# Performance work log

Hardware: AMD Instinct MI355X
Metric: run time of the kernel (lower is better)

Reference implementation:

```python
import jax, jax.numpy as jnp
import numpy as np

N_NODES = 100000
N_EDGES = 1250000
D_IN = 32
H = 64
EPS = 1e-5


def layer_norm(x, g, b):
    mu = jnp.mean(x, axis=-1, keepdims=True)
    var = jnp.mean(jnp.square(x - mu), axis=-1, keepdims=True)
    return (x - mu) * jax.lax.rsqrt(var + EPS) * g + b


def setup_inputs() -> dict:
    key = jax.random.key(0)
    ks = jax.random.split(key, 6)
    x = jax.random.normal(ks[0], (N_NODES, D_IN), dtype=jnp.float32)
    edge_index = jax.random.randint(ks[1], (2, N_EDGES), 0, N_NODES, dtype=jnp.int64)
    W1 = jax.random.normal(ks[2], (D_IN, H), dtype=jnp.float32) * (1.0 / np.sqrt(D_IN))
    b1 = jax.random.normal(ks[3], (H,), dtype=jnp.float32) * 0.01
    W2 = jax.random.normal(ks[4], (H, H), dtype=jnp.float32) * (1.0 / np.sqrt(H))
    b2 = jax.random.normal(ks[5], (H,), dtype=jnp.float32) * 0.01
    g1 = jnp.ones((H,), dtype=jnp.float32)
    beta1 = jnp.zeros((H,), dtype=jnp.float32)
    g2 = jnp.ones((H,), dtype=jnp.float32)
    beta2 = jnp.zeros((H,), dtype=jnp.float32)
    return {"x": x, "edge_index": edge_index, "W1": W1, "b1": b1, "g1": g1,
            "beta1": beta1, "W2": W2, "b2": b2, "g2": g2, "beta2": beta2}


def reference(x, edge_index, W1, b1, g1, beta1, W2, b2, g2, beta2):
    # node MLP: Linear -> LN -> ReLU, twice
    h = jax.nn.relu(layer_norm(x @ W1 + b1, g1, beta1))
    h = jax.nn.relu(layer_norm(h @ W2 + b2, g2, beta2))
    # message passing: gather source features, scatter-add to destinations
    row, col = edge_index[0], edge_index[1]
    aggr = jax.ops.segment_sum(h[col], row, num_segments=N_NODES)  # [N, H]
    return h + aggr
```

## Files before the change

kernel.cpp:

```cpp
#include <hip/hip_runtime.h>

#define N_NODES 100000
#define D_IN 32
#define H 64
#define EPS 1e-5f
#define RSTR 32
#define CAP 32
#define OV_CAP 32768

typedef float floatx2 __attribute__((ext_vector_type(2)));

__device__ __forceinline__ unsigned short f2bf(float f) {
    union { float f; unsigned int u; } c; c.f = f;
    unsigned int b = c.u + 0x7FFFu + ((c.u >> 16) & 1u);
    return (unsigned short)(b >> 16);
}
__device__ __forceinline__ float bf2f(unsigned short s) {
    union { unsigned int u; float f; } c; c.u = ((unsigned int)s) << 16;
    return c.f;
}

__global__ __launch_bounds__(256, 2) void fused_kernel(
    const float* __restrict__ x,
    const float* __restrict__ W1, const float* __restrict__ b1,
    const float* __restrict__ g1, const float* __restrict__ be1,
    const float* __restrict__ W2, const float* __restrict__ b2,
    const float* __restrict__ g2, const float* __restrict__ be2,
    unsigned short* __restrict__ hb, unsigned char* __restrict__ hb8,
    const int* __restrict__ ei, int* __restrict__ cnt, int* __restrict__ bkt,
    int* __restrict__ ovCnt, int2* __restrict__ ov,
    int E, int SB, int TOT)
{
    const int i = blockIdx.x;
    const int before = (int)((long long)i * SB / TOT);
    const int after  = (int)((long long)(i + 1) * SB / TOT);

    if (after > before) {
        int t = before * 256 + threadIdx.x;
        int e0 = t * 8;
        if (e0 >= E) return;

        int rows[8], cols[8], pos[8];
        if (e0 + 7 < E) {
            int4 r0 = *(const int4*)(ei + e0);
            int4 r1 = *(const int4*)(ei + e0 + 4);
            int4 c0 = *(const int4*)(ei + E + e0);
            int4 c1 = *(const int4*)(ei + E + e0 + 4);
            rows[0]=r0.x; rows[1]=r0.y; rows[2]=r0.z; rows[3]=r0.w;
            rows[4]=r1.x; rows[5]=r1.y; rows[6]=r1.z; rows[7]=r1.w;
            cols[0]=c0.x; cols[1]=c0.y; cols[2]=c0.z; cols[3]=c0.w;
            cols[4]=c1.x; cols[5]=c1.y; cols[6]=c1.z; cols[7]=c1.w;
        } else {
#pragma unroll
            for (int j = 0; j < 8; ++j) {
                int e = e0 + j;
                if (e < E) { rows[j] = ei[e]; cols[j] = ei[E + e]; }
                else rows[j] = -1;
            }
        }
#pragma unroll
        for (int j = 0; j < 8; ++j)
            if (rows[j] >= 0) pos[j] = atomicAdd(&cnt[rows[j]], 1);
#pragma unroll
        for (int j = 0; j < 8; ++j) {
            if (rows[j] < 0) continue;
            if (pos[j] < CAP) {
                __builtin_nontemporal_store(cols[j], &bkt[rows[j] * RSTR + pos[j]]);
            } else {
                int s = atomicAdd(ovCnt, 1);
                if (s < OV_CAP) ov[s] = make_int2(rows[j], cols[j]);
            }
        }
        return;
    }

    int gid = (i - before) * 256 + threadIdx.x;
    int node = gid < N_NODES ? gid : N_NODES - 1;

    float xr[D_IN];
    {
        const float4* xp = (const float4*)(x + (long long)node * D_IN);
#pragma unroll
        for (int i2 = 0; i2 < D_IN / 4; ++i2) {
            float4 v = xp[i2];
            xr[4*i2+0] = v.x; xr[4*i2+1] = v.y; xr[4*i2+2] = v.z; xr[4*i2+3] = v.w;
        }
    }

    float h1[H];
#pragma unroll
    for (int jb = 0; jb < H / 4; ++jb) {
        float4 b = *(const float4*)(b1 + jb * 4);
        h1[4*jb+0] = b.x; h1[4*jb+1] = b.y; h1[4*jb+2] = b.z; h1[4*jb+3] = b.w;
    }
#pragma unroll
    for (int k = 0; k < D_IN; ++k) {
        float xk = xr[k];
#pragma unroll
        for (int jb = 0; jb < H / 4; ++jb) {
            float4 w = *(const float4*)(W1 + k * H + jb * 4);
            h1[4*jb+0] += xk * w.x; h1[4*jb+1] += xk * w.y;
            h1[4*jb+2] += xk * w.z; h1[4*jb+3] += xk * w.w;
        }
    }
    {
        float s0=0,s1=0,s2=0,s3=0, q0=0,q1=0,q2=0,q3=0;
#pragma unroll
        for (int j = 0; j < H; j += 4) {
            s0 += h1[j+0]; s1 += h1[j+1]; s2 += h1[j+2]; s3 += h1[j+3];
            q0 += h1[j+0]*h1[j+0]; q1 += h1[j+1]*h1[j+1];
            q2 += h1[j+2]*h1[j+2]; q3 += h1[j+3]*h1[j+3];
        }
        float mu  = (s0+s1+s2+s3) * (1.0f / H);
        float var = (q0+q1+q2+q3) * (1.0f / H) - mu * mu;
        float rs  = rsqrtf(var + EPS);
#pragma unroll
        for (int jb = 0; jb < H / 4; ++jb) {
            float4 g = *(const float4*)(g1 + jb * 4);
            float4 be = *(const float4*)(be1 + jb * 4);
            h1[4*jb+0] = fmaxf((h1[4*jb+0]-mu)*rs*g.x + be.x, 0.0f);
            h1[4*jb+1] = fmaxf((h1[4*jb+1]-mu)*rs*g.y + be.y, 0.0f);
            h1[4*jb+2] = fmaxf((h1[4*jb+2]-mu)*rs*g.z + be.z, 0.0f);
            h1[4*jb+3] = fmaxf((h1[4*jb+3]-mu)*rs*g.w + be.w, 0.0f);
        }
    }

    float h2[H];
#pragma unroll
    for (int jb = 0; jb < H / 4; ++jb) {
        float4 b = *(const float4*)(b2 + jb * 4);
        h2[4*jb+0] = b.x; h2[4*jb+1] = b.y; h2[4*jb+2] = b.z; h2[4*jb+3] = b.w;
    }
#pragma unroll
    for (int k = 0; k < H; ++k) {
        float hk = h1[k];
#pragma unroll
        for (int jb = 0; jb < H / 4; ++jb) {
            float4 w = *(const float4*)(W2 + k * H + jb * 4);
            h2[4*jb+0] += hk * w.x; h2[4*jb+1] += hk * w.y;
            h2[4*jb+2] += hk * w.z; h2[4*jb+3] += hk * w.w;
        }
    }
    {
        float s0=0,s1=0,s2=0,s3=0, q0=0,q1=0,q2=0,q3=0;
#pragma unroll
        for (int j = 0; j < H; j += 4) {
            s0 += h2[j+0]; s1 += h2[j+1]; s2 += h2[j+2]; s3 += h2[j+3];
            q0 += h2[j+0]*h2[j+0]; q1 += h2[j+1]*h2[j+1];
            q2 += h2[j+2]*h2[j+2]; q3 += h2[j+3]*h2[j+3];
        }
        float mu  = (s0+s1+s2+s3) * (1.0f / H);
        float var = (q0+q1+q2+q3) * (1.0f / H) - mu * mu;
        float rs  = rsqrtf(var + EPS);

        unsigned short* hp = hb + (long long)node * H;
        unsigned int w8[H / 4];
#pragma unroll
        for (int jb = 0; jb < H / 4; ++jb) {
            float4 g = *(const float4*)(g2 + jb * 4);
            float4 be = *(const float4*)(be2 + jb * 4);
            float4 v;
            v.x = fmaxf((h2[4*jb+0]-mu)*rs*g.x + be.x, 0.0f);
            v.y = fmaxf((h2[4*jb+1]-mu)*rs*g.y + be.y, 0.0f);
            v.z = fmaxf((h2[4*jb+2]-mu)*rs*g.z + be.z, 0.0f);
            v.w = fmaxf((h2[4*jb+3]-mu)*rs*g.w + be.w, 0.0f);
            ushort4 u;
            u.x = f2bf(v.x); u.y = f2bf(v.y); u.z = f2bf(v.z); u.w = f2bf(v.w);
            *(ushort4*)(hp + 4*jb) = u;
            int lo = __builtin_amdgcn_cvt_pk_fp8_f32(v.x, v.y, 0, false);
            w8[jb] = (unsigned int)__builtin_amdgcn_cvt_pk_fp8_f32(v.z, v.w, lo, true);
        }
        unsigned int* hp8 = (unsigned int*)(hb8 + (long long)node * H);
#pragma unroll
        for (int q = 0; q < H / 16; ++q)
            *(uint4*)(hp8 + q * 4) = make_uint4(w8[4*q+0], w8[4*q+1], w8[4*q+2], w8[4*q+3]);
    }
}

__global__ __launch_bounds__(256, 2) void aggr_kernel(
    const int* __restrict__ cnt, const int* __restrict__ bkt,
    const unsigned short* __restrict__ hb, const unsigned char* __restrict__ hb8,
    float* __restrict__ out,
    const int* __restrict__ ovCnt, const int2* __restrict__ ov)
{
    const int t    = threadIdx.x & 63;
    const int sub  = t >> 4;
    const int l    = t & 15;
    const int q    = l & 3;
    const int g    = l >> 2;
    const int wave = blockIdx.x * 4 + (threadIdx.x >> 6);
    const int node = wave * 4 + sub;

    int m = cnt[node];
    if (m > CAP) m = CAP;
    const int base = node * RSTR;

    int4 ea = *(const int4*)(bkt + base + g * 8);
    int4 eb = *(const int4*)(bkt + base + g * 8 + 4);
    int ed[8] = { ea.x, ea.y, ea.z, ea.w, eb.x, eb.y, eb.z, eb.w };

    const uint4* h84 = (const uint4*)hb8;
    const int e0 = g * 8;

    float s[16];
#pragma unroll
    for (int j = 0; j < 16; ++j) s[j] = 0.f;

    uint4 vv[8];
#pragma unroll
    for (int k = 0; k < 8; ++k)
        if (e0 + k < m) vv[k] = h84[(ed[k] << 2) + q];

#pragma unroll
    for (int k = 0; k < 8; ++k) {
        if (e0 + k < m) {
            unsigned int w[4] = { vv[k].x, vv[k].y, vv[k].z, vv[k].w };
#pragma unroll
            for (int u = 0; u < 4; ++u) {
                floatx2 p0 = __builtin_amdgcn_cvt_pk_f32_fp8(w[u], false);
                floatx2 p1 = __builtin_amdgcn_cvt_pk_f32_fp8(w[u], true);
                s[4*u+0] += p0.x; s[4*u+1] += p0.y;
                s[4*u+2] += p1.x; s[4*u+3] += p1.y;
            }
        }
    }

#pragma unroll
    for (int j = 0; j < 16; ++j) {
        s[j] += __shfl_xor(s[j], 4, 64);
        s[j] += __shfl_xor(s[j], 8, 64);
    }

    const int co = q * 16 + g * 4;
    float a0 = s[g*4+0], a1 = s[g*4+1], a2 = s[g*4+2], a3 = s[g*4+3];

    {
        uint2 sv = *(const uint2*)(hb + ((long long)node << 6) + co);
        a0 += bf2f((unsigned short)(sv.x & 0xFFFFu));
        a1 += bf2f((unsigned short)(sv.x >> 16));
        a2 += bf2f((unsigned short)(sv.y & 0xFFFFu));
        a3 += bf2f((unsigned short)(sv.y >> 16));
    }

    int nov = *ovCnt; if (nov > OV_CAP) nov = OV_CAP;
    for (int i = 0; i < nov; ++i) {
        int2 rc = ov[i];
        if (rc.x == node) {
            uint2 vvо = *(const uint2*)(hb + ((long long)rc.y << 6) + co);
            a0 += bf2f((unsigned short)(vvо.x & 0xFFFFu));
            a1 += bf2f((unsigned short)(vvо.x >> 16));
            a2 += bf2f((unsigned short)(vvо.y & 0xFFFFu));
            a3 += bf2f((unsigned short)(vvо.y >> 16));
        }
    }

    *(float4*)(out + ((long long)node << 6) + co) = make_float4(a0, a1, a2, a3);
}

extern "C" void kernel_launch(void* const* d_in, const int* in_sizes, int n_in,
                              void* d_out, int out_size, void* d_ws, size_t ws_size,
                              hipStream_t stream)
{
    const float* x   = (const float*)d_in[0];
    const int*   ei  = (const int*)d_in[1];
    const float* W1  = (const float*)d_in[2];
    const float* b1  = (const float*)d_in[3];
    const float* g1  = (const float*)d_in[4];
    const float* be1 = (const float*)d_in[5];
    const float* W2  = (const float*)d_in[6];
    const float* b2  = (const float*)d_in[7];
    const float* g2  = (const float*)d_in[8];
    const float* be2 = (const float*)d_in[9];

    float* out = (float*)d_out;

    char* ws = (char*)d_ws;
    unsigned short* hb    = (unsigned short*)ws;
    unsigned char*  hb8   = (unsigned char*)(ws + 12800000);
    int*            cnt   = (int*)(ws + 19200000);
    int*            ovCnt = (int*)(ws + 19600000);
    int2*           ov    = (int2*)(ws + 19600064);
    int*            bkt   = (int*)(ws + 19862208);

    const int E = in_sizes[1] / 2;

    (void)hipMemsetAsync(cnt, 0, 400064, stream);

    const int SB = ((E + 7) / 8 + 255) / 256;
    const int MB = (N_NODES + 255) / 256;
    fused_kernel<<<SB + MB, 256, 0, stream>>>(
        x, W1, b1, g1, be1, W2, b2, g2, be2, hb, hb8,
        ei, cnt, bkt, ovCnt, ov, E, SB, SB + MB);

    aggr_kernel<<<N_NODES / 16, 256, 0, stream>>>(cnt, bkt, hb, hb8, out, ovCnt, ov);
}
```

Baseline: 205.9 us.

## Split aggregation into two source-range passes to shrink gathered working set

Aggregation now runs as two launches. Each launch gathers only edges whose source node falls in half of the node range, so the fp8 feature table being read randomly is about half as large per pass and is more likely to stay cache-resident. The first pass writes partial sums plus the self term to the output. The second pass reads those back and adds the other half and the overflow edges. In exchange, the bucket lists are read twice, the output makes an extra write and read round trip, and there is a second launch.

```diff
diff --git a/kernel.cpp b/kernel.cpp
--- a/kernel.cpp
+++ b/kernel.cpp
@@ -7,6 +7,7 @@
 #define RSTR 32
 #define CAP 32
 #define OV_CAP 32768
+#define SRC_HALF 50000
 
 typedef float floatx2 __attribute__((ext_vector_type(2)));
 
@@ -177,11 +178,12 @@
     }
 }
 
-__global__ __launch_bounds__(256, 2) void aggr_kernel(
+__global__ __launch_bounds__(256, 2) void aggr_pass_kernel(
     const int* __restrict__ cnt, const int* __restrict__ bkt,
     const unsigned short* __restrict__ hb, const unsigned char* __restrict__ hb8,
     float* __restrict__ out,
-    const int* __restrict__ ovCnt, const int2* __restrict__ ov)
+    const int* __restrict__ ovCnt, const int2* __restrict__ ov,
+    int srcLo, int srcHi, int isFinal)
 {
     const int t    = threadIdx.x & 63;
     const int sub  = t >> 4;
@@ -198,9 +200,14 @@
     int4 ea = *(const int4*)(bkt + base + g * 8);
     int4 eb = *(const int4*)(bkt + base + g * 8 + 4);
     int ed[8] = { ea.x, ea.y, ea.z, ea.w, eb.x, eb.y, eb.z, eb.w };
+    const int e0 = g * 8;
+
+    bool keep[8];
+#pragma unroll
+    for (int k = 0; k < 8; ++k)
+        keep[k] = (e0 + k < m) && (ed[k] >= srcLo) && (ed[k] < srcHi);
 
     const uint4* h84 = (const uint4*)hb8;
-    const int e0 = g * 8;
 
     float s[16];
 #pragma unroll
@@ -209,11 +216,11 @@
     uint4 vv[8];
 #pragma unroll
     for (int k = 0; k < 8; ++k)
-        if (e0 + k < m) vv[k] = h84[(ed[k] << 2) + q];
+        if (keep[k]) vv[k] = h84[(ed[k] << 2) + q];
 
 #pragma unroll
     for (int k = 0; k < 8; ++k) {
-        if (e0 + k < m) {
+        if (keep[k]) {
             unsigned int w[4] = { vv[k].x, vv[k].y, vv[k].z, vv[k].w };
 #pragma unroll
             for (int u = 0; u < 4; ++u) {
@@ -234,23 +241,26 @@
     const int co = q * 16 + g * 4;
     float a0 = s[g*4+0], a1 = s[g*4+1], a2 = s[g*4+2], a3 = s[g*4+3];
 
-    {
+    if (!isFinal) {
         uint2 sv = *(const uint2*)(hb + ((long long)node << 6) + co);
         a0 += bf2f((unsigned short)(sv.x & 0xFFFFu));
         a1 += bf2f((unsigned short)(sv.x >> 16));
         a2 += bf2f((unsigned short)(sv.y & 0xFFFFu));
         a3 += bf2f((unsigned short)(sv.y >> 16));
-    }
-
-    int nov = *ovCnt; if (nov > OV_CAP) nov = OV_CAP;
-    for (int i = 0; i < nov; ++i) {
-        int2 rc = ov[i];
-        if (rc.x == node) {
-            uint2 vvо = *(const uint2*)(hb + ((long long)rc.y << 6) + co);
-            a0 += bf2f((unsigned short)(vvо.x & 0xFFFFu));
-            a1 += bf2f((unsigned short)(vvо.x >> 16));
-            a2 += bf2f((unsigned short)(vvо.y & 0xFFFFu));
-            a3 += bf2f((unsigned short)(vvо.y >> 16));
+    } else {
+        float4 prev = *(const float4*)(out + ((long long)node << 6) + co);
+        a0 += prev.x; a1 += prev.y; a2 += prev.z; a3 += prev.w;
+
+        int nov = *ovCnt; if (nov > OV_CAP) nov = OV_CAP;
+        for (int i = 0; i < nov; ++i) {
+            int2 rc = ov[i];
+            if (rc.x == node) {
+                uint2 vo = *(const uint2*)(hb + ((long long)rc.y << 6) + co);
+                a0 += bf2f((unsigned short)(vo.x & 0xFFFFu));
+                a1 += bf2f((unsigned short)(vo.x >> 16));
+                a2 += bf2f((unsigned short)(vo.y & 0xFFFFu));
+                a3 += bf2f((unsigned short)(vo.y >> 16));
+            }
         }
     }
 
@@ -292,5 +302,8 @@
         x, W1, b1, g1, be1, W2, b2, g2, be2, hb, hb8,
         ei, cnt, bkt, ovCnt, ov, E, SB, SB + MB);
 
-    aggr_kernel<<<N_NODES / 16, 256, 0, stream>>>(cnt, bkt, hb, hb8, out, ovCnt, ov);
-}
+    aggr_pass_kernel<<<N_NODES / 16, 256, 0, stream>>>(
+        cnt, bkt, hb, hb8, out, ovCnt, ov, 0, SRC_HALF, 0);
+    aggr_pass_kernel<<<N_NODES / 16, 256, 0, stream>>>(
+        cnt, bkt, hb, hb8, out, ovCnt, ov, SRC_HALF, N_NODES, 1);
+}
```

Measured after the change: 222.5 us. 8.1% more time.

## Split edge bucketing by destination half to overlap with aggregation

Applied to the files above, without the earlier changes.

Edge bucketing is split by destination-row range into two passes. The first pass (rows below 50000) runs alongside the node MLP. The second pass (upper rows) runs in the same kernel that aggregates the lower half of nodes, and a third kernel aggregates the upper half. This is meant to overlap scatter atomics with gather work and shorten the dependency chain; in exchange the full edge list is read twice and one more kernel launch is added. Lower-half aggregation reads the overflow count while upper-half scatter may still be appending entries, which could pick up stale overflow records.

```diff
diff --git a/kernel.cpp b/kernel.cpp
--- a/kernel.cpp
+++ b/kernel.cpp
@@ -7,6 +7,7 @@
 #define RSTR 32
 #define CAP 32
 #define OV_CAP 32768
+#define HALF 50000
 
 typedef float floatx2 __attribute__((ext_vector_type(2)));
 
@@ -20,7 +21,130 @@
     return c.f;
 }
 
-__global__ __launch_bounds__(256, 2) void fused_kernel(
+__device__ __forceinline__ void scatter_range(
+    const int* __restrict__ ei, int* __restrict__ cnt, int* __restrict__ bkt,
+    int* __restrict__ ovCnt, int2* __restrict__ ov,
+    int E, int chunk, int lo, int hi)
+{
+    int t = chunk * 256 + threadIdx.x;
+    int e0 = t * 8;
+    if (e0 >= E) return;
+
+    int rows[8], cols[8], pos[8];
+    if (e0 + 7 < E) {
+        int4 r0 = *(const int4*)(ei + e0);
+        int4 r1 = *(const int4*)(ei + e0 + 4);
+        int4 c0 = *(const int4*)(ei + E + e0);
+        int4 c1 = *(const int4*)(ei + E + e0 + 4);
+        rows[0]=r0.x; rows[1]=r0.y; rows[2]=r0.z; rows[3]=r0.w;
+        rows[4]=r1.x; rows[5]=r1.y; rows[6]=r1.z; rows[7]=r1.w;
+        cols[0]=c0.x; cols[1]=c0.y; cols[2]=c0.z; cols[3]=c0.w;
+        cols[4]=c1.x; cols[5]=c1.y; cols[6]=c1.z; cols[7]=c1.w;
+    } else {
+#pragma unroll
+        for (int j = 0; j < 8; ++j) {
+            int e = e0 + j;
+            if (e < E) { rows[j] = ei[e]; cols[j] = ei[E + e]; }
+            else rows[j] = -1;
+        }
+    }
+#pragma unroll
+    for (int j = 0; j < 8; ++j) {
+        pos[j] = -1;
+        if (rows[j] >= lo && rows[j] < hi)
+            pos[j] = atomicAdd(&cnt[rows[j]], 1);
+    }
+#pragma unroll
+    for (int j = 0; j < 8; ++j) {
+        if (pos[j] < 0) continue;
+        if (pos[j] < CAP) {
+            __builtin_nontemporal_store(cols[j], &bkt[rows[j] * RSTR + pos[j]]);
+        } else {
+            int s = atomicAdd(ovCnt, 1);
+            if (s < OV_CAP) ov[s] = make_int2(rows[j], cols[j]);
+        }
+    }
+}
+
+__device__ __forceinline__ void aggr_node(
+    const int* __restrict__ cnt, const int* __restrict__ bkt,
+    const unsigned short* __restrict__ hb, const unsigned char* __restrict__ hb8,
+    float* __restrict__ out,
+    const int* __restrict__ ovCnt, const int2* __restrict__ ov,
+    int node)
+{
+    const int t = threadIdx.x & 63;
+    const int l = t & 15;
+    const int q = l & 3;
+    const int g = l >> 2;
+
+    int m = cnt[node];
+    if (m > CAP) m = CAP;
+    const int base = node * RSTR;
+
+    int4 ea = *(const int4*)(bkt + base + g * 8);
+    int4 eb = *(const int4*)(bkt + base + g * 8 + 4);
+    int ed[8] = { ea.x, ea.y, ea.z, ea.w, eb.x, eb.y, eb.z, eb.w };
+    const int e0 = g * 8;
+
+    const uint4* h84 = (const uint4*)hb8;
+
+    float s[16];
+#pragma unroll
+    for (int j = 0; j < 16; ++j) s[j] = 0.f;
+
+    uint4 vv[8];
+#pragma unroll
+    for (int k = 0; k < 8; ++k)
+        if (e0 + k < m) vv[k] = h84[(ed[k] << 2) + q];
+
+#pragma unroll
+    for (int k = 0; k < 8; ++k) {
+        if (e0 + k < m) {
+            unsigned int w[4] = { vv[k].x, vv[k].y, vv[k].z, vv[k].w };
+#pragma unroll
+            for (int u = 0; u < 4; ++u) {
+                floatx2 p0 = __builtin_amdgcn_cvt_pk_f32_fp8(w[u], false);
+                floatx2 p1 = __builtin_amdgcn_cvt_pk_f32_fp8(w[u], true);
+                s[4*u+0] += p0.x; s[4*u+1] += p0.y;
+                s[4*u+2] += p1.x; s[4*u+3] += p1.y;
+            }
+        }
+    }
+
+#pragma unroll
+    for (int j = 0; j < 16; ++j) {
+        s[j] += __shfl_xor(s[j], 4, 64);
+        s[j] += __shfl_xor(s[j], 8, 64);
+    }
+
+    const int co = q * 16 + g * 4;
+    float a0 = s[g*4+0], a1 = s[g*4+1], a2 = s[g*4+2], a3 = s[g*4+3];
+
+    {
+        uint2 sv = *(const uint2*)(hb + ((long long)node << 6) + co);
+        a0 += bf2f((unsigned short)(sv.x & 0xFFFFu));
+        a1 += bf2f((unsigned short)(sv.x >> 16));
+        a2 += bf2f((unsigned short)(sv.y & 0xFFFFu));
+        a3 += bf2f((unsigned short)(sv.y >> 16));
+    }
+
+    int nov = *ovCnt; if (nov > OV_CAP) nov = OV_CAP;
+    for (int i = 0; i < nov; ++i) {
+        int2 rc = ov[i];
+        if (rc.x == node) {
+            uint2 vo = *(const uint2*)(hb + ((long long)rc.y << 6) + co);
+            a0 += bf2f((unsigned short)(vo.x & 0xFFFFu));
+            a1 += bf2f((unsigned short)(vo.x >> 16));
+            a2 += bf2f((unsigned short)(vo.y & 0xFFFFu));
+            a3 += bf2f((unsigned short)(vo.y >> 16));
+        }
+    }
+
+    *(float4*)(out + ((long long)node << 6) + co) = make_float4(a0, a1, a2, a3);
+}
+
+__global__ __launch_bounds__(256, 2) void k1_kernel(
     const float* __restrict__ x,
     const float* __restrict__ W1, const float* __restrict__ b1,
     const float* __restrict__ g1, const float* __restrict__ be1,
@@ -36,41 +160,7 @@
     const int after  = (int)((long long)(i + 1) * SB / TOT);
 
     if (after > before) {
-        int t = before * 256 + threadIdx.x;
-        int e0 = t * 8;
-        if (e0 >= E) return;
-
-        int rows[8], cols[8], pos[8];
-        if (e0 + 7 < E) {
-            int4 r0 = *(const int4*)(ei + e0);
-            int4 r1 = *(const int4*)(ei + e0 + 4);
-            int4 c0 = *(const int4*)(ei + E + e0);
-            int4 c1 = *(const int4*)(ei + E + e0 + 4);
-            rows[0]=r0.x; rows[1]=r0.y; rows[2]=r0.z; rows[3]=r0.w;
-            rows[4]=r1.x; rows[5]=r1.y; rows[6]=r1.z; rows[7]=r1.w;
-            cols[0]=c0.x; cols[1]=c0.y; cols[2]=c0.z; cols[3]=c0.w;
-            cols[4]=c1.x; cols[5]=c1.y; cols[6]=c1.z; cols[7]=c1.w;
-        } else {
-#pragma unroll
-            for (int j = 0; j < 8; ++j) {
-                int e = e0 + j;
-                if (e < E) { rows[j] = ei[e]; cols[j] = ei[E + e]; }
-                else rows[j] = -1;
-            }
-        }
-#pragma unroll
-        for (int j = 0; j < 8; ++j)
-            if (rows[j] >= 0) pos[j] = atomicAdd(&cnt[rows[j]], 1);
-#pragma unroll
-        for (int j = 0; j < 8; ++j) {
-            if (rows[j] < 0) continue;
-            if (pos[j] < CAP) {
-                __builtin_nontemporal_store(cols[j], &bkt[rows[j] * RSTR + pos[j]]);
-            } else {
-                int s = atomicAdd(ovCnt, 1);
-                if (s < OV_CAP) ov[s] = make_int2(rows[j], cols[j]);
-            }
-        }
+        scatter_range(ei, cnt, bkt, ovCnt, ov, E, before, 0, HALF);
         return;
     }
 
@@ -177,7 +267,30 @@
     }
 }
 
-__global__ __launch_bounds__(256, 2) void aggr_kernel(
+__global__ __launch_bounds__(256, 2) void k2_kernel(
+    const unsigned short* __restrict__ hb, const unsigned char* __restrict__ hb8,
+    const int* __restrict__ ei, int* __restrict__ cnt, int* __restrict__ bkt,
+    int* __restrict__ ovCnt, int2* __restrict__ ov,
+    float* __restrict__ out,
+    int E, int SB, int TOT)
+{
+    const int i = blockIdx.x;
+    const int before = (int)((long long)i * SB / TOT);
+    const int after  = (int)((long long)(i + 1) * SB / TOT);
+
+    if (after > before) {
+        scatter_range(ei, cnt, bkt, ovCnt, ov, E, before, HALF, N_NODES);
+        return;
+    }
+
+    const int t    = threadIdx.x & 63;
+    const int sub  = t >> 4;
+    const int wave = (i - before) * 4 + (threadIdx.x >> 6);
+    const int node = wave * 4 + sub;
+    aggr_node(cnt, bkt, hb, hb8, out, ovCnt, ov, node);
+}
+
+__global__ __launch_bounds__(256, 2) void k3_kernel(
     const int* __restrict__ cnt, const int* __restrict__ bkt,
     const unsigned short* __restrict__ hb, const unsigned char* __restrict__ hb8,
     float* __restrict__ out,
@@ -185,76 +298,9 @@
 {
     const int t    = threadIdx.x & 63;
     const int sub  = t >> 4;
-    const int l    = t & 15;
-    const int q    = l & 3;
-    const int g    = l >> 2;
     const int wave = blockIdx.x * 4 + (threadIdx.x >> 6);
-    const int node = wave * 4 + sub;
-
-    int m = cnt[node];
-    if (m > CAP) m = CAP;
-    const int base = node * RSTR;
-
-    int4 ea = *(const int4*)(bkt + base + g * 8);
-    int4 eb = *(const int4*)(bkt + base + g * 8 + 4);
-    int ed[8] = { ea.x, ea.y, ea.z, ea.w, eb.x, eb.y, eb.z, eb.w };
-
-    const uint4* h84 = (const uint4*)hb8;
-    const int e0 = g * 8;
-
-    float s[16];
-#pragma unroll
-    for (int j = 0; j < 16; ++j) s[j] = 0.f;
-
-    uint4 vv[8];
-#pragma unroll
-    for (int k = 0; k < 8; ++k)
-        if (e0 + k < m) vv[k] = h84[(ed[k] << 2) + q];
-
-#pragma unroll
-    for (int k = 0; k < 8; ++k) {
-        if (e0 + k < m) {
-            unsigned int w[4] = { vv[k].x, vv[k].y, vv[k].z, vv[k].w };
-#pragma unroll
-            for (int u = 0; u < 4; ++u) {
-                floatx2 p0 = __builtin_amdgcn_cvt_pk_f32_fp8(w[u], false);
-                floatx2 p1 = __builtin_amdgcn_cvt_pk_f32_fp8(w[u], true);
-                s[4*u+0] += p0.x; s[4*u+1] += p0.y;
-                s[4*u+2] += p1.x; s[4*u+3] += p1.y;
-            }
-        }
-    }
-
-#pragma unroll
-    for (int j = 0; j < 16; ++j) {
-        s[j] += __shfl_xor(s[j], 4, 64);
-        s[j] += __shfl_xor(s[j], 8, 64);
-    }
-
-    const int co = q * 16 + g * 4;
-    float a0 = s[g*4+0], a1 = s[g*4+1], a2 = s[g*4+2], a3 = s[g*4+3];
-
-    {
-        uint2 sv = *(const uint2*)(hb + ((long long)node << 6) + co);
-        a0 += bf2f((unsigned short)(sv.x & 0xFFFFu));
-        a1 += bf2f((unsigned short)(sv.x >> 16));
-        a2 += bf2f((unsigned short)(sv.y & 0xFFFFu));
-        a3 += bf2f((unsigned short)(sv.y >> 16));
-    }
-
-    int nov = *ovCnt; if (nov > OV_CAP) nov = OV_CAP;
-    for (int i = 0; i < nov; ++i) {
-        int2 rc = ov[i];
-        if (rc.x == node) {
-            uint2 vvо = *(const uint2*)(hb + ((long long)rc.y << 6) + co);
-            a0 += bf2f((unsigned short)(vvо.x & 0xFFFFu));
-            a1 += bf2f((unsigned short)(vvо.x >> 16));
-            a2 += bf2f((unsigned short)(vvо.y & 0xFFFFu));
-            a3 += bf2f((unsigned short)(vvо.y >> 16));
-        }
-    }
-
-    *(float4*)(out + ((long long)node << 6) + co) = make_float4(a0, a1, a2, a3);
+    const int node = HALF + wave * 4 + sub;
+    aggr_node(cnt, bkt, hb, hb8, out, ovCnt, ov, node);
 }
 
 extern "C" void kernel_launch(void* const* d_in, const int* in_sizes, int n_in,
@@ -286,11 +332,16 @@
 
     (void)hipMemsetAsync(cnt, 0, 400064, stream);
 
-    const int SB = ((E + 7) / 8 + 255) / 256;
-    const int MB = (N_NODES + 255) / 256;
-    fused_kernel<<<SB + MB, 256, 0, stream>>>(
+    const int SB  = ((E + 7) / 8 + 255) / 256;
+    const int MB  = (N_NODES + 255) / 256;
+    const int AB  = HALF / 16;
+
+    k1_kernel<<<SB + MB, 256, 0, stream>>>(
         x, W1, b1, g1, be1, W2, b2, g2, be2, hb, hb8,
         ei, cnt, bkt, ovCnt, ov, E, SB, SB + MB);
 
-    aggr_kernel<<<N_NODES / 16, 256, 0, stream>>>(cnt, bkt, hb, hb8, out, ovCnt, ov);
-}
+    k2_kernel<<<SB + AB, 256, 0, stream>>>(
+        hb, hb8, ei, cnt, bkt, ovCnt, ov, out, E, SB, SB + AB);
+
+    k3_kernel<<<AB, 256, 0, stream>>>(cnt, bkt, hb, hb8, out, ovCnt, ov);
+}
```

Measured after the change: 212.0 us. 3.0% more time.

## Replace global per-row atomic bucketing with two-pass binned partition via shared memory

Applied to the files above, without the earlier changes.

Edges are first partitioned into 196 coarse bins of 512 rows, using shared-memory histograms and one global atomic per bin per block. They are written as packed (local row, col) words. A new kernel then builds each bin's per-row buckets in LDS and streams them out coalesced. This replaces 1.25M scattered global atomics and scattered bucket stores, at the cost of an extra kernel launch, an extra pass over the partition buffer, and a large LDS footprint (about 66KB per block) that limits occupancy of the new kernel.

```diff
diff --git a/kernel.cpp b/kernel.cpp
--- a/kernel.cpp
+++ b/kernel.cpp
@@ -7,6 +7,9 @@
 #define RSTR 32
 #define CAP 32
 #define OV_CAP 32768
+#define NBINS 196
+#define BINSZ 512
+#define BINCAP 7168
 
 typedef float floatx2 __attribute__((ext_vector_type(2)));
 
@@ -20,14 +23,14 @@
     return c.f;
 }
 
-__global__ __launch_bounds__(256, 2) void fused_kernel(
+__global__ __launch_bounds__(256, 2) void ka_kernel(
     const float* __restrict__ x,
     const float* __restrict__ W1, const float* __restrict__ b1,
     const float* __restrict__ g1, const float* __restrict__ be1,
     const float* __restrict__ W2, const float* __restrict__ b2,
     const float* __restrict__ g2, const float* __restrict__ be2,
     unsigned short* __restrict__ hb, unsigned char* __restrict__ hb8,
-    const int* __restrict__ ei, int* __restrict__ cnt, int* __restrict__ bkt,
+    const int* __restrict__ ei, int* __restrict__ part, int* __restrict__ binCur,
     int* __restrict__ ovCnt, int2* __restrict__ ov,
     int E, int SB, int TOT)
 {
@@ -36,11 +39,13 @@
     const int after  = (int)((long long)(i + 1) * SB / TOT);
 
     if (after > before) {
+        __shared__ int hist[NBINS];
+        __shared__ int basev[NBINS];
+
         int t = before * 256 + threadIdx.x;
         int e0 = t * 8;
-        if (e0 >= E) return;
-
-        int rows[8], cols[8], pos[8];
+
+        int rows[8], cols[8], myofs[8];
         if (e0 + 7 < E) {
             int4 r0 = *(const int4*)(ei + e0);
             int4 r1 = *(const int4*)(ei + e0 + 4);
@@ -58,14 +63,28 @@
                 else rows[j] = -1;
             }
         }
+
+        if (threadIdx.x < NBINS) hist[threadIdx.x] = 0;
+        __syncthreads();
+
 #pragma unroll
         for (int j = 0; j < 8; ++j)
-            if (rows[j] >= 0) pos[j] = atomicAdd(&cnt[rows[j]], 1);
+            if (rows[j] >= 0) myofs[j] = atomicAdd(&hist[rows[j] >> 9], 1);
+        __syncthreads();
+
+        if (threadIdx.x < NBINS) {
+            int h = hist[threadIdx.x];
+            if (h > 0) basev[threadIdx.x] = atomicAdd(&binCur[threadIdx.x], h);
+        }
+        __syncthreads();
+
 #pragma unroll
         for (int j = 0; j < 8; ++j) {
             if (rows[j] < 0) continue;
-            if (pos[j] < CAP) {
-                __builtin_nontemporal_store(cols[j], &bkt[rows[j] * RSTR + pos[j]]);
+            int bin  = rows[j] >> 9;
+            int slot = basev[bin] + myofs[j];
+            if (slot < BINCAP) {
+                part[bin * BINCAP + slot] = ((rows[j] & (BINSZ - 1)) << 17) | cols[j];
             } else {
                 int s = atomicAdd(ovCnt, 1);
                 if (s < OV_CAP) ov[s] = make_int2(rows[j], cols[j]);
@@ -177,6 +196,48 @@
     }
 }
 
+__global__ __launch_bounds__(256, 2) void kb_kernel(
+    const int* __restrict__ part, const int* __restrict__ binCur,
+    int* __restrict__ cnt, int* __restrict__ bkt,
+    int* __restrict__ ovCnt, int2* __restrict__ ov)
+{
+    __shared__ int cnt_l[BINSZ];
+    __shared__ int bkt_l[BINSZ * CAP];
+
+    const int bin = blockIdx.x;
+    int n = binCur[bin];
+    if (n > BINCAP) n = BINCAP;
+    const int gbase = bin << 9;
+
+    for (int r = threadIdx.x; r < BINSZ; r += 256) cnt_l[r] = 0;
+    __syncthreads();
+
+    const int* p = part + bin * BINCAP;
+    for (int idx = threadIdx.x; idx < n; idx += 256) {
+        int v = p[idx];
+        int r = v >> 17;
+        int c = v & 0x1FFFF;
+        int pos = atomicAdd(&cnt_l[r], 1);
+        if (pos < CAP) {
+            bkt_l[r * CAP + pos] = c;
+        } else {
+            int s = atomicAdd(ovCnt, 1);
+            if (s < OV_CAP) ov[s] = make_int2(gbase + r, c);
+        }
+    }
+    __syncthreads();
+
+    uint4* gb = (uint4*)bkt;
+    const uint4* lb = (const uint4*)bkt_l;
+    for (int idx = threadIdx.x; idx < BINSZ * 8; idx += 256) {
+        int row = idx >> 3;
+        if (gbase + row < N_NODES)
+            gb[(long long)(gbase + row) * 8 + (idx & 7)] = lb[idx];
+    }
+    for (int r = threadIdx.x; r < BINSZ; r += 256)
+        if (gbase + r < N_NODES) cnt[gbase + r] = cnt_l[r];
+}
+
 __global__ __launch_bounds__(256, 2) void aggr_kernel(
     const int* __restrict__ cnt, const int* __restrict__ bkt,
     const unsigned short* __restrict__ hb, const unsigned char* __restrict__ hb8,
@@ -198,9 +259,9 @@
     int4 ea = *(const int4*)(bkt + base + g * 8);
     int4 eb = *(const int4*)(bkt + base + g * 8 + 4);
     int ed[8] = { ea.x, ea.y, ea.z, ea.w, eb.x, eb.y, eb.z, eb.w };
+    const int e0 = g * 8;
 
     const uint4* h84 = (const uint4*)hb8;
-    const int e0 = g * 8;
 
     float s[16];
 #pragma unroll
@@ -246,11 +307,11 @@
     for (int i = 0; i < nov; ++i) {
         int2 rc = ov[i];
         if (rc.x == node) {
-            uint2 vvо = *(const uint2*)(hb + ((long long)rc.y << 6) + co);
-            a0 += bf2f((unsigned short)(vvо.x & 0xFFFFu));
-            a1 += bf2f((unsigned short)(vvо.x >> 16));
-            a2 += bf2f((unsigned short)(vvо.y & 0xFFFFu));
-            a3 += bf2f((unsigned short)(vvо.y >> 16));
+            uint2 vo = *(const uint2*)(hb + ((long long)rc.y << 6) + co);
+            a0 += bf2f((unsigned short)(vo.x & 0xFFFFu));
+            a1 += bf2f((unsigned short)(vo.x >> 16));
+            a2 += bf2f((unsigned short)(vo.y & 0xFFFFu));
+            a3 += bf2f((unsigned short)(vo.y >> 16));
         }
     }
 
@@ -275,22 +336,27 @@
     float* out = (float*)d_out;
 
     char* ws = (char*)d_ws;
-    unsigned short* hb    = (unsigned short*)ws;
-    unsigned char*  hb8   = (unsigned char*)(ws + 12800000);
-    int*            cnt   = (int*)(ws + 19200000);
-    int*            ovCnt = (int*)(ws + 19600000);
-    int2*           ov    = (int2*)(ws + 19600064);
-    int*            bkt   = (int*)(ws + 19862208);
+    unsigned short* hb     = (unsigned short*)ws;
+    unsigned char*  hb8    = (unsigned char*)(ws + 12800000);
+    int*            cnt    = (int*)(ws + 19200000);
+    int*            ovCnt  = (int*)(ws + 19600000);
+    int2*           ov     = (int2*)(ws + 19600064);
+    int*            binCur = (int*)(ws + 19862208);
+    int*            bkt    = (int*)(ws + 19863040);
+    int*            part   = (int*)(ws + 32663040);
 
     const int E = in_sizes[1] / 2;
 
-    (void)hipMemsetAsync(cnt, 0, 400064, stream);
+    (void)hipMemsetAsync(ws + 19600000, 0, 263040, stream);
 
     const int SB = ((E + 7) / 8 + 255) / 256;
     const int MB = (N_NODES + 255) / 256;
-    fused_kernel<<<SB + MB, 256, 0, stream>>>(
+
+    ka_kernel<<<SB + MB, 256, 0, stream>>>(
         x, W1, b1, g1, be1, W2, b2, g2, be2, hb, hb8,
-        ei, cnt, bkt, ovCnt, ov, E, SB, SB + MB);
+        ei, part, binCur, ovCnt, ov, E, SB, SB + MB);
+
+    kb_kernel<<<NBINS, 256, 0, stream>>>(part, binCur, cnt, bkt, ovCnt, ov);
 
     aggr_kernel<<<N_NODES / 16, 256, 0, stream>>>(cnt, bkt, hb, hb8, out, ovCnt, ov);
 }
```

Measured after the change: 188.2 us. -8.6%, faster.
